# Optimization experiments

Measured on AMD Instinct MI355X. Metric: run time of the kernel, lower is better.

Reference implementation:

```python
import math
import jax, jax.numpy as jnp
import numpy as np

POS_DIM = 32


def _fourier_features(pos, dim):
    # pos: [B, M] in [0,1] -> [B, M, dim]
    half = dim // 2
    freqs = jnp.exp(jnp.linspace(0.0, math.log(1000.0), half, dtype=pos.dtype))
    ang = pos[..., None] * freqs                      # [B, M, half]
    out = jnp.concatenate([jnp.sin(ang), jnp.cos(ang)], axis=-1)
    if out.shape[-1] < dim:  # pad if dim is odd (not the case for dim=32)
        pad = jnp.zeros(out.shape[:-1] + (dim - out.shape[-1],), dtype=pos.dtype)
        out = jnp.concatenate([out, pad], axis=-1)
    return out


def setup_inputs() -> dict:
    key = jax.random.key(0)
    k1, k2, k3 = jax.random.split(key, 3)
    B, T, D, M = 8, 8192, 512, 512
    frame_emb = jax.random.normal(k1, (B, T, D), dtype=jnp.float32)
    beat_bounds = jax.random.randint(k2, (B, M, 2), 0, T).astype(jnp.int64)
    # nn.Linear(D + POS_DIM, D): store as [in, out] for x @ W + b
    bound = 1.0 / math.sqrt(D + POS_DIM)
    W = jax.random.uniform(k3, (D + POS_DIM, D), dtype=jnp.float32,
                           minval=-bound, maxval=bound)
    b = jnp.zeros((D,), dtype=jnp.float32)
    return {"frame_emb": frame_emb, "beat_bounds": beat_bounds, "W": W, "b": b}


def reference(frame_emb, beat_bounds, W, b):
    B, T, D = frame_emb.shape
    M = beat_bounds.shape[1]
    dt = frame_emb.dtype

    # clamp bounds exactly as the torch loop does
    s = jnp.clip(beat_bounds[..., 0], 0, T - 1)                 # [B, M]
    e = jnp.maximum(s + 1, jnp.minimum(beat_bounds[..., 1], T))  # [B, M]

    # segment mean via exclusive cumsum: sum(frame_emb[b, s:e]) = cs[e] - cs[s]
    cs = jnp.concatenate(
        [jnp.zeros((B, 1, D), dtype=dt), jnp.cumsum(frame_emb, axis=1)], axis=1
    )  # [B, T+1, D]
    seg_sum = (jnp.take_along_axis(cs, e[..., None], axis=1)
               - jnp.take_along_axis(cs, s[..., None], axis=1))   # [B, M, D]
    counts = (e - s).astype(dt)[..., None]
    out = seg_sum / counts

    # fourier position features over beat index
    pos = (jnp.arange(M, dtype=dt) / max(1, M - 1)).clip(0.0, 1.0)  # [M]
    ff = _fourier_features(jnp.broadcast_to(pos[None, :], (B, M)), POS_DIM)
    out = jnp.concatenate([out, ff], axis=-1) @ W + b               # [B, M, D]
    return out
```

## Files before the change

kernel.cpp:

```cpp
#include <hip/hip_runtime.h>
#include <math.h>

#define B 8
#define T 8192
#define D 512
#define M 512
#define POS 32
#define KIN (D + POS)
#define CHUNK 16
#define NCHUNK (T / CHUNK)
#define GRP 16
#define NGRP (NCHUNK / GRP)
#define BM (B * M)

__global__ __launch_bounds__(128) void k_chunksum(const float* __restrict__ fe,
                                                  float* __restrict__ cp) {
    int blk = blockIdx.x;
    int b = blk / NCHUNK;
    int c = blk % NCHUNK;
    int d4 = threadIdx.x << 2;
    const float* src = fe + ((size_t)(b * T + c * CHUNK) * D + d4);
    float4 acc = {0.f, 0.f, 0.f, 0.f};
#pragma unroll
    for (int r = 0; r < CHUNK; ++r) {
        float4 v = *(const float4*)(src + (size_t)r * D);
        acc.x += v.x; acc.y += v.y; acc.z += v.z; acc.w += v.w;
    }
    *(float4*)(cp + ((size_t)b * NCHUNK + c) * D + d4) = acc;
}

__global__ __launch_bounds__(128) void k_scan_fine(float* __restrict__ cp,
                                                   float* __restrict__ gsum) {
    int b = blockIdx.x / NGRP;
    int g = blockIdx.x % NGRP;
    int d4 = threadIdx.x << 2;
    float* base = cp + ((size_t)b * NCHUNK + (size_t)g * GRP) * D + d4;
    float4 acc = {0.f, 0.f, 0.f, 0.f};
#pragma unroll
    for (int k = 0; k < GRP; ++k) {
        float4 v = *(const float4*)(base + (size_t)k * D);
        acc.x += v.x; acc.y += v.y; acc.z += v.z; acc.w += v.w;
        *(float4*)(base + (size_t)k * D) = acc;
    }
    *(float4*)(gsum + ((size_t)b * NGRP + g) * D + d4) = acc;
}

__global__ __launch_bounds__(128) void k_scan_coarse(const float* __restrict__ gsum,
                                                     float* __restrict__ gx) {
    int b = blockIdx.x;
    int d4 = threadIdx.x << 2;
    float4 acc = {0.f, 0.f, 0.f, 0.f};
#pragma unroll
    for (int g = 0; g < NGRP; ++g) {
        *(float4*)(gx + ((size_t)b * (NGRP + 1) + g) * D + d4) = acc;
        float4 v = *(const float4*)(gsum + ((size_t)b * NGRP + g) * D + d4);
        acc.x += v.x; acc.y += v.y; acc.z += v.z; acc.w += v.w;
    }
    *(float4*)(gx + ((size_t)b * (NGRP + 1) + NGRP) * D + d4) = acc;
}

__global__ __launch_bounds__(128) void k_buildx(const float* __restrict__ fe,
                                                const int* __restrict__ bounds,
                                                const float* __restrict__ cp,
                                                const float* __restrict__ gx,
                                                float* __restrict__ X) {
    int bm = blockIdx.x;
    int b = bm / M;
    int m = bm % M;
    int b0 = bounds[bm * 2 + 0];
    int b1 = bounds[bm * 2 + 1];
    int s = min(max(b0, 0), T - 1);
    int e = max(min(b1, T), s + 1);
    int cs_ = s >> 4, ce = e >> 4;
    int d4 = threadIdx.x << 2;

    const float* cpb = cp + (size_t)b * NCHUNK * D;
    const float* gxb = gx + (size_t)b * (NGRP + 1) * D;

    float4 acc = *(const float4*)(gxb + (size_t)(ce >> 4) * D + d4);
    if (ce & 15) {
        float4 v = *(const float4*)(cpb + (size_t)(ce - 1) * D + d4);
        acc.x += v.x; acc.y += v.y; acc.z += v.z; acc.w += v.w;
    }
    {
        float4 p = *(const float4*)(gxb + (size_t)(cs_ >> 4) * D + d4);
        acc.x -= p.x; acc.y -= p.y; acc.z -= p.z; acc.w -= p.w;
        if (cs_ & 15) {
            float4 v = *(const float4*)(cpb + (size_t)(cs_ - 1) * D + d4);
            acc.x -= v.x; acc.y -= v.y; acc.z -= v.z; acc.w -= v.w;
        }
    }

    const float* feb = fe + (size_t)b * T * D + d4;
    for (int t = ce * CHUNK; t < e; ++t) {
        float4 v = *(const float4*)(feb + (size_t)t * D);
        acc.x += v.x; acc.y += v.y; acc.z += v.z; acc.w += v.w;
    }
    for (int t = cs_ * CHUNK; t < s; ++t) {
        float4 v = *(const float4*)(feb + (size_t)t * D);
        acc.x -= v.x; acc.y -= v.y; acc.z -= v.z; acc.w -= v.w;
    }
    float inv = 1.0f / (float)(e - s);
    acc.x *= inv; acc.y *= inv; acc.z *= inv; acc.w *= inv;

    float* xr = X + (size_t)bm * KIN;
    *(float4*)(xr + d4) = acc;

    int t = threadIdx.x;
    if (t < POS) {
        int i = t & 15;
        float freq = expf(0.46051701859880914f * (float)i);
        float pos = (float)m * (1.0f / 511.0f);
        float ang = pos * freq;
        xr[D + t] = (t < 16) ? sinf(ang) : cosf(ang);
    }
}

#define TM 128
#define TN 64
#define TKc 16
__global__ __launch_bounds__(256) void k_gemm(const float* __restrict__ X,
                                              const float* __restrict__ W,
                                              const float* __restrict__ bias,
                                              float* __restrict__ out) {
    __shared__ float Xs[TKc][TM + 4];
    __shared__ float Ws[TKc][TN + 4];
    int n0 = blockIdx.x * TN;
    int m0 = blockIdx.y * TM;
    int tid = threadIdx.x;
    int tx = tid & 15, ty = tid >> 4;

    float acc[8][4] = {{0.f}};

    for (int k0 = 0; k0 < KIN; k0 += TKc) {
        {
            int row = tid >> 1;
            int kq = (tid & 1) << 3;
            const float* xp = X + (size_t)(m0 + row) * KIN + k0 + kq;
            float4 v0 = *(const float4*)xp;
            float4 v1 = *(const float4*)(xp + 4);
            Xs[kq + 0][row] = v0.x; Xs[kq + 1][row] = v0.y;
            Xs[kq + 2][row] = v0.z; Xs[kq + 3][row] = v0.w;
            Xs[kq + 4][row] = v1.x; Xs[kq + 5][row] = v1.y;
            Xs[kq + 6][row] = v1.z; Xs[kq + 7][row] = v1.w;
            float4 w = *(const float4*)(W + (size_t)(k0 + ty) * D + n0 + (tx << 2));
            *(float4*)&Ws[ty][tx << 2] = w;
        }
        __syncthreads();
#pragma unroll
        for (int k = 0; k < TKc; ++k) {
            float4 a0 = *(const float4*)&Xs[k][ty << 3];
            float4 a1 = *(const float4*)&Xs[k][(ty << 3) + 4];
            float4 w4 = *(const float4*)&Ws[k][tx << 2];
            acc[0][0] += a0.x * w4.x; acc[0][1] += a0.x * w4.y; acc[0][2] += a0.x * w4.z; acc[0][3] += a0.x * w4.w;
            acc[1][0] += a0.y * w4.x; acc[1][1] += a0.y * w4.y; acc[1][2] += a0.y * w4.z; acc[1][3] += a0.y * w4.w;
            acc[2][0] += a0.z * w4.x; acc[2][1] += a0.z * w4.y; acc[2][2] += a0.z * w4.z; acc[2][3] += a0.z * w4.w;
            acc[3][0] += a0.w * w4.x; acc[3][1] += a0.w * w4.y; acc[3][2] += a0.w * w4.z; acc[3][3] += a0.w * w4.w;
            acc[4][0] += a1.x * w4.x; acc[4][1] += a1.x * w4.y; acc[4][2] += a1.x * w4.z; acc[4][3] += a1.x * w4.w;
            acc[5][0] += a1.y * w4.x; acc[5][1] += a1.y * w4.y; acc[5][2] += a1.y * w4.z; acc[5][3] += a1.y * w4.w;
            acc[6][0] += a1.z * w4.x; acc[6][1] += a1.z * w4.y; acc[6][2] += a1.z * w4.z; acc[6][3] += a1.z * w4.w;
            acc[7][0] += a1.w * w4.x; acc[7][1] += a1.w * w4.y; acc[7][2] += a1.w * w4.z; acc[7][3] += a1.w * w4.w;
        }
        __syncthreads();
    }

    float4 bv = *(const float4*)(bias + n0 + (tx << 2));
#pragma unroll
    for (int i = 0; i < 8; ++i) {
        float4 o;
        o.x = acc[i][0] + bv.x;
        o.y = acc[i][1] + bv.y;
        o.z = acc[i][2] + bv.z;
        o.w = acc[i][3] + bv.w;
        *(float4*)(out + (size_t)(m0 + (ty << 3) + i) * D + n0 + (tx << 2)) = o;
    }
}

extern "C" void kernel_launch(void* const* d_in, const int* in_sizes, int n_in,
                              void* d_out, int out_size, void* d_ws, size_t ws_size,
                              hipStream_t stream) {
    const float* fe = (const float*)d_in[0];
    const int* bounds = (const int*)d_in[1];
    const float* W = (const float*)d_in[2];
    const float* bias = (const float*)d_in[3];
    float* out = (float*)d_out;

    float* cp = (float*)d_ws;
    float* gsum = cp + (size_t)B * NCHUNK * D;
    float* gx = gsum + (size_t)B * NGRP * D;
    float* X = gx + (size_t)B * (NGRP + 1) * D;

    k_chunksum<<<B * NCHUNK, 128, 0, stream>>>(fe, cp);
    k_scan_fine<<<B * NGRP, 128, 0, stream>>>(cp, gsum);
    k_scan_coarse<<<B, 128, 0, stream>>>(gsum, gx);
    k_buildx<<<BM, 128, 0, stream>>>(fe, bounds, cp, gx, X);
    dim3 g(D / TN, BM / TM);
    k_gemm<<<g, 256, 0, stream>>>(X, W, bias, out);
}
```

Measured before the change: 282.2 us.

## Fuse chunk sum with fine scan and shrink GEMM M-tile to 64

Merges the chunk-sum and fine-scan kernels into one kernel that streams 256 rows per block and writes running prefix chunks directly. This removes a launch and the read-modify-write pass over the chunk buffer. The fused kernel launches only 512 blocks of 64 threads to read the whole 128MB input, so the memory system may be underused. The GEMM tile shrinks from 128 to 64 rows, doubling the number of blocks at the cost of less register reuse per thread.

```diff
diff --git a/kernel.cpp b/kernel.cpp
--- a/kernel.cpp
+++ b/kernel.cpp
@@ -13,34 +13,27 @@
 #define NGRP (NCHUNK / GRP)
 #define BM (B * M)
 
-__global__ __launch_bounds__(128) void k_chunksum(const float* __restrict__ fe,
-                                                  float* __restrict__ cp) {
+__global__ __launch_bounds__(64) void k_scanchunk(const float* __restrict__ fe,
+                                                  float* __restrict__ cp,
+                                                  float* __restrict__ gsum) {
     int blk = blockIdx.x;
-    int b = blk / NCHUNK;
-    int c = blk % NCHUNK;
-    int d4 = threadIdx.x << 2;
-    const float* src = fe + ((size_t)(b * T + c * CHUNK) * D + d4);
+    int b = blk >> 6;
+    int g = (blk >> 1) & 31;
+    int h = blk & 1;
+    int d4 = (h << 8) + (threadIdx.x << 2);
+
+    const float* src = fe + ((size_t)(b * T + g * (GRP * CHUNK)) * D + d4);
+    float* cpb = cp + ((size_t)b * NCHUNK + (size_t)g * GRP) * D + d4;
+
     float4 acc = {0.f, 0.f, 0.f, 0.f};
+#pragma unroll 2
+    for (int c = 0; c < GRP; ++c) {
 #pragma unroll
-    for (int r = 0; r < CHUNK; ++r) {
-        float4 v = *(const float4*)(src + (size_t)r * D);
-        acc.x += v.x; acc.y += v.y; acc.z += v.z; acc.w += v.w;
-    }
-    *(float4*)(cp + ((size_t)b * NCHUNK + c) * D + d4) = acc;
-}
-
-__global__ __launch_bounds__(128) void k_scan_fine(float* __restrict__ cp,
-                                                   float* __restrict__ gsum) {
-    int b = blockIdx.x / NGRP;
-    int g = blockIdx.x % NGRP;
-    int d4 = threadIdx.x << 2;
-    float* base = cp + ((size_t)b * NCHUNK + (size_t)g * GRP) * D + d4;
-    float4 acc = {0.f, 0.f, 0.f, 0.f};
-#pragma unroll
-    for (int k = 0; k < GRP; ++k) {
-        float4 v = *(const float4*)(base + (size_t)k * D);
-        acc.x += v.x; acc.y += v.y; acc.z += v.z; acc.w += v.w;
-        *(float4*)(base + (size_t)k * D) = acc;
+        for (int r = 0; r < CHUNK; ++r) {
+            float4 v = *(const float4*)(src + (size_t)(c * CHUNK + r) * D);
+            acc.x += v.x; acc.y += v.y; acc.z += v.z; acc.w += v.w;
+        }
+        *(float4*)(cpb + (size_t)c * D) = acc;
     }
     *(float4*)(gsum + ((size_t)b * NGRP + g) * D + d4) = acc;
 }
@@ -116,7 +109,7 @@
     }
 }
 
-#define TM 128
+#define TM 64
 #define TN 64
 #define TKc 16
 __global__ __launch_bounds__(256) void k_gemm(const float* __restrict__ X,
@@ -130,49 +123,42 @@
     int tid = threadIdx.x;
     int tx = tid & 15, ty = tid >> 4;
 
-    float acc[8][4] = {{0.f}};
+    float acc[4][4] = {{0.f}};
 
     for (int k0 = 0; k0 < KIN; k0 += TKc) {
         {
-            int row = tid >> 1;
-            int kq = (tid & 1) << 3;
-            const float* xp = X + (size_t)(m0 + row) * KIN + k0 + kq;
-            float4 v0 = *(const float4*)xp;
-            float4 v1 = *(const float4*)(xp + 4);
-            Xs[kq + 0][row] = v0.x; Xs[kq + 1][row] = v0.y;
-            Xs[kq + 2][row] = v0.z; Xs[kq + 3][row] = v0.w;
-            Xs[kq + 4][row] = v1.x; Xs[kq + 5][row] = v1.y;
-            Xs[kq + 6][row] = v1.z; Xs[kq + 7][row] = v1.w;
+            int row = tid >> 2;
+            int kq = (tid & 3) << 2;
+            float4 v = *(const float4*)(X + (size_t)(m0 + row) * KIN + k0 + kq);
+            Xs[kq + 0][row] = v.x;
+            Xs[kq + 1][row] = v.y;
+            Xs[kq + 2][row] = v.z;
+            Xs[kq + 3][row] = v.w;
             float4 w = *(const float4*)(W + (size_t)(k0 + ty) * D + n0 + (tx << 2));
             *(float4*)&Ws[ty][tx << 2] = w;
         }
         __syncthreads();
 #pragma unroll
         for (int k = 0; k < TKc; ++k) {
-            float4 a0 = *(const float4*)&Xs[k][ty << 3];
-            float4 a1 = *(const float4*)&Xs[k][(ty << 3) + 4];
+            float4 a = *(const float4*)&Xs[k][ty << 2];
             float4 w4 = *(const float4*)&Ws[k][tx << 2];
-            acc[0][0] += a0.x * w4.x; acc[0][1] += a0.x * w4.y; acc[0][2] += a0.x * w4.z; acc[0][3] += a0.x * w4.w;
-            acc[1][0] += a0.y * w4.x; acc[1][1] += a0.y * w4.y; acc[1][2] += a0.y * w4.z; acc[1][3] += a0.y * w4.w;
-            acc[2][0] += a0.z * w4.x; acc[2][1] += a0.z * w4.y; acc[2][2] += a0.z * w4.z; acc[2][3] += a0.z * w4.w;
-            acc[3][0] += a0.w * w4.x; acc[3][1] += a0.w * w4.y; acc[3][2] += a0.w * w4.z; acc[3][3] += a0.w * w4.w;
-            acc[4][0] += a1.x * w4.x; acc[4][1] += a1.x * w4.y; acc[4][2] += a1.x * w4.z; acc[4][3] += a1.x * w4.w;
-            acc[5][0] += a1.y * w4.x; acc[5][1] += a1.y * w4.y; acc[5][2] += a1.y * w4.z; acc[5][3] += a1.y * w4.w;
-            acc[6][0] += a1.z * w4.x; acc[6][1] += a1.z * w4.y; acc[6][2] += a1.z * w4.z; acc[6][3] += a1.z * w4.w;
-            acc[7][0] += a1.w * w4.x; acc[7][1] += a1.w * w4.y; acc[7][2] += a1.w * w4.z; acc[7][3] += a1.w * w4.w;
+            acc[0][0] += a.x * w4.x; acc[0][1] += a.x * w4.y; acc[0][2] += a.x * w4.z; acc[0][3] += a.x * w4.w;
+            acc[1][0] += a.y * w4.x; acc[1][1] += a.y * w4.y; acc[1][2] += a.y * w4.z; acc[1][3] += a.y * w4.w;
+            acc[2][0] += a.z * w4.x; acc[2][1] += a.z * w4.y; acc[2][2] += a.z * w4.z; acc[2][3] += a.z * w4.w;
+            acc[3][0] += a.w * w4.x; acc[3][1] += a.w * w4.y; acc[3][2] += a.w * w4.z; acc[3][3] += a.w * w4.w;
         }
         __syncthreads();
     }
 
     float4 bv = *(const float4*)(bias + n0 + (tx << 2));
 #pragma unroll
-    for (int i = 0; i < 8; ++i) {
+    for (int i = 0; i < 4; ++i) {
         float4 o;
         o.x = acc[i][0] + bv.x;
         o.y = acc[i][1] + bv.y;
         o.z = acc[i][2] + bv.z;
         o.w = acc[i][3] + bv.w;
-        *(float4*)(out + (size_t)(m0 + (ty << 3) + i) * D + n0 + (tx << 2)) = o;
+        *(float4*)(out + (size_t)(m0 + (ty << 2) + i) * D + n0 + (tx << 2)) = o;
     }
 }
 
@@ -190,8 +176,7 @@
     float* gx = gsum + (size_t)B * NGRP * D;
     float* X = gx + (size_t)B * (NGRP + 1) * D;
 
-    k_chunksum<<<B * NCHUNK, 128, 0, stream>>>(fe, cp);
-    k_scan_fine<<<B * NGRP, 128, 0, stream>>>(cp, gsum);
+    k_scanchunk<<<B * NGRP * 2, 64, 0, stream>>>(fe, cp, gsum);
     k_scan_coarse<<<B, 128, 0, stream>>>(gsum, gx);
     k_buildx<<<BM, 128, 0, stream>>>(fe, bounds, cp, gx, X);
     dim3 g(D / TN, BM / TM);
```

After: 267.9 us. 5.1% less time.
